# Optimization experiments

Measured on AMD Instinct MI355X. Metric: run time of the kernel, lower is better.

The kernel has to match this reference:

```python
import jax, jax.numpy as jnp
import numpy as np

H = 256   # d_model (SSM copies)
N = 32    # half state size (conjugate symmetry)
S = 256   # n_ssm (trainable copies); repeat = H//S = 1
R = 1     # low-rank correction rank
CCH = 32  # channels; must equal N for the final dC contraction
LMAX = 2048
BATCH = 2


def _r2c(x):
    return x[..., 0] + 1j * x[..., 1]


def setup_inputs() -> dict:
    key = jax.random.key(0)
    ks = jax.random.split(key, 8)
    # dt ~ loguniform(1e-3, 1e-1), standard S4 init
    log_dt = jnp.log(1e-3) + jax.random.uniform(ks[0], (H,), dtype=jnp.float32) * (jnp.log(1e-1) - jnp.log(1e-3))
    B_ri = 0.5 * jax.random.normal(ks[1], (1, S, N, 2), dtype=jnp.float32)
    P_ri = 0.5 * jax.random.normal(ks[2], (R, S, N, 2), dtype=jnp.float32)
    C_ri = 0.5 * jax.random.normal(ks[3], (CCH, H, N, 2), dtype=jnp.float32)
    # real_type='exp': w_real = -exp(inv_w_real) < 0 (stable poles)
    inv_w_real = 0.5 * jax.random.normal(ks[4], (S, N), dtype=jnp.float32)
    # HiPPO-style imaginary parts ~ pi * n, with small noise
    w_imag = jnp.pi * jnp.broadcast_to(jnp.arange(N, dtype=jnp.float32), (S, N)) + 0.01 * jax.random.normal(ks[5], (S, N), dtype=jnp.float32)
    dC = 0.1 * jax.random.normal(ks[6], (LMAX, H, N), dtype=jnp.float32)
    previous_decode = jax.random.normal(ks[7], (BATCH, H, LMAX), dtype=jnp.float32)
    return dict(log_dt=log_dt, B_ri=B_ri, P_ri=P_ri, C_ri=C_ri,
                inv_w_real=inv_w_real, w_imag=w_imag, dC=dC,
                previous_decode=previous_decode, L=LMAX)


def _ss_kernel(log_dt, B_ri, P_ri, C_ri, inv_w_real, w_imag, L):
    """NPLR SSM kernel K_L via Cauchy evaluation + rank-1 Woodbury + irfft. Returns (channels, H, L) real."""
    H_ = log_dt.shape[0]
    S_ = inv_w_real.shape[0]
    rep = H_ // S_
    dt = jnp.exp(log_dt)                              # (H,)
    B = _r2c(B_ri)                                    # (1, S, N)
    P = _r2c(P_ri)                                    # (R, S, N)
    C = _r2c(C_ri)                                    # (CCH, H, N)
    Q = jnp.conj(P)
    w = -jnp.exp(inv_w_real) + 1j * w_imag            # (S, N), real_type='exp'
    # FFT nodes (roots of unity) and bilinear-transformed nodes
    Lf = L // 2 + 1
    omega = jnp.exp((-2j * jnp.pi / L) * jnp.arange(Lf, dtype=jnp.float32))  # (Lf,)
    z = 2 * (1 - omega) / (1 + omega)                 # (Lf,)
    # broadcast S -> H ('r t n -> r (v t) n')
    B = jnp.tile(B, (1, rep, 1))                      # (1, H, N)
    P = jnp.tile(P, (1, rep, 1))                      # (R, H, N)
    Q = jnp.tile(Q, (1, rep, 1))
    w = jnp.tile(w, (rep, 1)) * dt[:, None]           # (H, N) : w * dt
    Bc = jnp.concatenate([B, P], axis=0)              # (1+R, H, N)
    Cc = jnp.concatenate([C, Q], axis=0)              # (CCH+R, H, N)
    v = Bc[:, None] * Cc[None]                        # (1+R, CCH+R, H, N)
    # conjugate-symmetric Cauchy kernel: sum_n v/(z-w) + conj(v)/(z-conj(w))
    cau_p = 1.0 / (z[None, None, :] - w[:, :, None])              # (H, N, Lf)
    cau_m = 1.0 / (z[None, None, :] - jnp.conj(w)[:, :, None])    # (H, N, Lf)
    r = jnp.einsum('ijhn,hnl->ijhl', v, cau_p) + jnp.einsum('ijhn,hnl->ijhl', jnp.conj(v), cau_m)
    r = r * dt[None, None, :, None]
    # rank-1 Woodbury correction
    k_f = r[:-1, :-1] - r[:-1, -1:] * r[-1:, :-1] / (1 + r[-1:, -1:])  # (1, CCH, H, Lf)
    k_f = k_f * 2 / (1 + omega)
    k = jnp.fft.irfft(k_f, n=L, axis=-1)              # (1, CCH, H, L) real
    return k[-1]                                      # (CCH, H, L)


def reference(log_dt, B_ri, P_ri, C_ri, inv_w_real, w_imag, dC, previous_decode, L):
    k = _ss_kernel(log_dt, B_ri, P_ri, C_ri, inv_w_real, w_imag, L)  # (CCH, H, L)
    # FFT convolution of previous_decode with the kernel (length-2L, linear conv)
    k_f = jnp.fft.rfft(k, n=2 * L, axis=-1)                          # (CCH, H, L+1)
    pd_f = jnp.fft.rfft(previous_decode, n=2 * L, axis=-1)           # (B, H, L+1)
    x_f = jnp.einsum('bhl,chl->bhcl', pd_f, k_f)                     # (B, H, CCH, L+1)
    x_pred = jnp.fft.irfft(x_f, n=2 * L, axis=-1)[..., :L]           # (B, H, CCH, L)
    out = jnp.einsum('bhnl,lhn->bhl', x_pred, dC)                    # (B, H, L)
    return out
```

## Files before the change

### kernel.cpp

```cpp
#include <hip/hip_runtime.h>
#include <math.h>

#define LF   1025

#define OFF_ZT   65536
#define OFF_KF   131072
#define OFF_PDF  67371008
#define OFF_DCT  84148224

__device__ __forceinline__ float2 cmulf(float2 a, float2 b){
    return make_float2(a.x*b.x - a.y*b.y, a.x*b.y + a.y*b.x);
}

__device__ __forceinline__ float2 twid(float r){
    float s, c;
    asm("v_sin_f32 %0, %1" : "=v"(s) : "v"(r));
    asm("v_cos_f32 %0, %1" : "=v"(c) : "v"(r));
    return make_float2(c, -s);
}
__device__ __forceinline__ float frcp(float x){
    float y; asm("v_rcp_f32 %0, %1" : "=v"(y) : "v"(x)); return y;
}
__device__ __forceinline__ void lds_fence(){
    asm volatile("s_waitcnt lgkmcnt(0)" ::: "memory");
}

#define GS 548
__device__ __forceinline__ int gslot(int g, int s){ return g*GS + s + (s >> 4); }
__device__ __forceinline__ int binslot(int j){ return gslot(j & 3, j >> 2); }

__global__ void initk(float4* __restrict__ ZT){
    int i = blockIdx.x*256 + threadIdx.x;
    if (i < LF){
        double th = (-2.0*M_PI) * (double)i / 2048.0;
        double cr = cos(th), ci = sin(th);
        double ar = 1.0 + cr, ai = ci;
        double den = ar*ar + ai*ai;
        double nr = 1.0 - cr, ni = -ci;
        double zr = 2.0*(nr*ar + ni*ai)/den;
        double zi = 2.0*(ni*ar - nr*ai)/den;
        ZT[i] = make_float4((float)zr, (float)zi, (float)(2.0*ar/den), (float)(-2.0*ai/den));
    }
}

__global__ __launch_bounds__(256) void transpose_dC(const float* __restrict__ dC, float* __restrict__ DCT){
    __shared__ float tile[32][260];
    int hc0 = blockIdx.x*32;
    int l0  = blockIdx.y*256;
    int tx = threadIdx.x;
    int ty = threadIdx.y;
    for (int li = ty; li < 256; li += 8)
        tile[tx][li] = dC[(size_t)(l0+li)*8192 + hc0 + tx];
    __syncthreads();
    for (int i = ty; i < 32; i += 8){
        #pragma unroll
        for (int pk = 0; pk < 256; pk += 32){
            int po = pk + tx;
            int ll = ((po & 63) << 2) | (po >> 6);
            DCT[(size_t)(hc0+i)*2048 + l0 + po] = tile[i][ll];
        }
    }
}

__global__ __launch_bounds__(256,2) void cauchy_k(
                         const float* __restrict__ log_dt, const float* __restrict__ B_ri,
                         const float* __restrict__ P_ri, const float* __restrict__ C_ri,
                         const float* __restrict__ ivw, const float* __restrict__ wimag,
                         const float4* __restrict__ ZT, float2* __restrict__ KF)
{
    const int h  = blockIdx.y;
    const int c0 = blockIdx.z * 16;
    const int l  = blockIdx.x*256 + (int)threadIdx.x;
    __shared__ float2 wv[32], bv[32], pv[32];
    __shared__ float2 cc[16][32];
    __shared__ float dt_sh;
    if (threadIdx.x < 32){
        int n = threadIdx.x;
        float dt = expf(log_dt[h]);
        wv[n] = make_float2(-expf(ivw[h*32+n]) * dt, wimag[h*32+n] * dt);
        bv[n] = make_float2(B_ri[(h*32+n)*2+0], B_ri[(h*32+n)*2+1]);
        pv[n] = make_float2(P_ri[(h*32+n)*2+0], P_ri[(h*32+n)*2+1]);
        if (n == 0) dt_sh = dt;
    }
    #pragma unroll
    for (int k2 = 0; k2 < 2; ++k2){
        int i = threadIdx.x + k2*256;
        int cj = i >> 5, n = i & 31;
        size_t base = (((size_t)(c0+cj)*256 + h)*32 + n)*2;
        cc[cj][n] = make_float2(C_ri[base+0], C_ri[base+1]);
    }
    __syncthreads();
    if (l >= LF) return;

    float4 zt = ZT[l];
    const float zx = zt.x, zy = zt.y;
    float r0x[17], r0y[17], r1x[17], r1y[17];
    #pragma unroll
    for (int j=0;j<17;++j){ r0x[j]=0.f; r0y[j]=0.f; r1x[j]=0.f; r1y[j]=0.f; }

    #pragma unroll 1
    for (int n=0; n<32; ++n){
        float2 wn = wv[n];
        float dx = zx - wn.x;
        float dy = zy - wn.y;
        float ey = zy + wn.y;
        float ip = frcp(dx*dx + dy*dy);
        float im = frcp(dx*dx + ey*ey);
        float cpx = dx*ip, cpy = -dy*ip;
        float cmx = dx*im, cmy = -ey*im;
        float2 bn = bv[n];
        float br = bn.x, bi = bn.y;
        float t0x = br*cpx - bi*cpy, t0y = br*cpy + bi*cpx;
        float t1x = br*cmx + bi*cmy, t1y = br*cmy - bi*cmx;
        float2 pn = pv[n];
        float pr = pn.x, pi = pn.y;
        float t2x = pr*cpx - pi*cpy, t2y = pr*cpy + pi*cpx;
        float t3x = pr*cmx + pi*cmy, t3y = pr*cmy - pi*cmx;
        float u0 = t0x+t1x, v0 = t1y-t0y, s0 = t0y+t1y, q0 = t0x-t1x;
        float u1 = t2x+t3x, v1 = t3y-t2y, s1 = t2y+t3y, q1 = t2x-t3x;
        r0x[16] = fmaf(pr,u0, fmaf(-pi,v0, r0x[16]));
        r0y[16] = fmaf(pr,s0, fmaf(-pi,q0, r0y[16]));
        r1x[16] = fmaf(pr,u1, fmaf(-pi,v1, r1x[16]));
        r1y[16] = fmaf(pr,s1, fmaf(-pi,q1, r1y[16]));
        #pragma unroll
        for (int j=0;j<16;++j){
            float2 c = cc[j][n];
            float a = c.x, b = c.y;
            r0x[j] = fmaf(a,u0, fmaf(b,v0, r0x[j]));
            r0y[j] = fmaf(a,s0, fmaf(b,q0, r0y[j]));
            r1x[j] = fmaf(a,u1, fmaf(b,v1, r1x[j]));
            r1y[j] = fmaf(a,s1, fmaf(b,q1, r1y[j]));
        }
    }

    float dt = dt_sh;
    #pragma unroll
    for (int j=0;j<17;++j){ r0x[j]*=dt; r0y[j]*=dt; r1x[j]*=dt; r1y[j]*=dt; }
    float drr = 1.0f + r1x[16], dii = r1y[16];
    float idn = frcp(drr*drr + dii*dii);
    float gx = (r0x[16]*drr + r0y[16]*dii)*idn;
    float gy = (r0y[16]*drr - r0x[16]*dii)*idn;
    float tfx = zt.z, tfy = zt.w;
    #pragma unroll
    for (int j=0;j<16;++j){
        float kr = r0x[j] - (gx*r1x[j] - gy*r1y[j]);
        float ki = r0y[j] - (gx*r1y[j] + gy*r1x[j]);
        KF[((size_t)((c0+j)*256+h))*1026 + l] = make_float2(kr*tfx - ki*tfy, kr*tfy + ki*tfx);
    }
}

template<bool INV>
__device__ __forceinline__ void bfly8(float2 v[8]){
    float2 e0,e1,e2,e3,o0,o1,o2,o3;
    {
        float t0x=v[0].x+v[4].x, t0y=v[0].y+v[4].y;
        float t1x=v[0].x-v[4].x, t1y=v[0].y-v[4].y;
        float t2x=v[2].x+v[6].x, t2y=v[2].y+v[6].y;
        float t3x=v[2].x-v[6].x, t3y=v[2].y-v[6].y;
        e0 = make_float2(t0x+t2x, t0y+t2y);
        e2 = make_float2(t0x-t2x, t0y-t2y);
        if (!INV){ e1 = make_float2(t1x+t3y, t1y-t3x); e3 = make_float2(t1x-t3y, t1y+t3x); }
        else     { e1 = make_float2(t1x-t3y, t1y+t3x); e3 = make_float2(t1x+t3y, t1y-t3x); }
    }
    {
        float t0x=v[1].x+v[5].x, t0y=v[1].y+v[5].y;
        float t1x=v[1].x-v[5].x, t1y=v[1].y-v[5].y;
        float t2x=v[3].x+v[7].x, t2y=v[3].y+v[7].y;
        float t3x=v[3].x-v[7].x, t3y=v[3].y-v[7].y;
        o0 = make_float2(t0x+t2x, t0y+t2y);
        o2 = make_float2(t0x-t2x, t0y-t2y);
        if (!INV){ o1 = make_float2(t1x+t3y, t1y-t3x); o3 = make_float2(t1x-t3y, t1y+t3x); }
        else     { o1 = make_float2(t1x-t3y, t1y+t3x); o3 = make_float2(t1x+t3y, t1y-t3x); }
    }
    const float RC = 0.70710678118654752f;
    float2 w1o1, w2o2, w3o3;
    if (!INV){
        w1o1 = make_float2(RC*(o1.x+o1.y), RC*(o1.y-o1.x));
        w2o2 = make_float2(o2.y, -o2.x);
        w3o3 = make_float2(RC*(o3.y-o3.x), RC*(-o3.x-o3.y));
    } else {
        w1o1 = make_float2(RC*(o1.x-o1.y), RC*(o1.y+o1.x));
        w2o2 = make_float2(-o2.y, o2.x);
        w3o3 = make_float2(RC*(-o3.x-o3.y), RC*(o3.x-o3.y));
    }
    v[0] = make_float2(e0.x+o0.x,   e0.y+o0.y);
    v[1] = make_float2(e1.x+w1o1.x, e1.y+w1o1.y);
    v[2] = make_float2(e2.x+w2o2.x, e2.y+w2o2.y);
    v[3] = make_float2(e3.x+w3o3.x, e3.y+w3o3.y);
    v[4] = make_float2(e0.x-o0.x,   e0.y-o0.y);
    v[5] = make_float2(e1.x-w1o1.x, e1.y-w1o1.y);
    v[6] = make_float2(e2.x-w2o2.x, e2.y-w2o2.y);
    v[7] = make_float2(e3.x-w3o3.x, e3.y-w3o3.y);
}

template<bool INV, bool REGOUT>
__device__ __forceinline__ void fftR(float2 v[8], int r0, float2* __restrict__ A, float2* __restrict__ B){
    const int t = threadIdx.x;
    #pragma unroll
    for (int half=0; half<2; ++half){
        int r = r0 + half*256;
        float2 x0=v[half], x1=v[2+half], x2=v[4+half], x3=v[6+half];
        float t0x=x0.x+x2.x, t0y=x0.y+x2.y;
        float t1x=x0.x-x2.x, t1y=x0.y-x2.y;
        float t2x=x1.x+x3.x, t2y=x1.y+x3.y;
        float t3x=x1.x-x3.x, t3y=x1.y-x3.y;
        float2 y0 = make_float2(t0x+t2x, t0y+t2y);
        float2 y2 = make_float2(t0x-t2x, t0y-t2y);
        float2 y1, y3;
        if (!INV){ y1 = make_float2(t1x+t3y, t1y-t3x); y3 = make_float2(t1x-t3y, t1y+t3x); }
        else     { y1 = make_float2(t1x-t3y, t1y+t3x); y3 = make_float2(t1x+t3y, t1y-t3x); }
        float2 w1 = twid((float)r * (1.0f/2048.0f));
        if (INV) w1.y = -w1.y;
        float2 w2 = cmulf(w1,w1);
        float2 w3 = cmulf(w2,w1);
        A[gslot(0,r)] = y0;
        A[gslot(1,r)] = cmulf(y1,w1);
        A[gslot(2,r)] = cmulf(y2,w2);
        A[gslot(3,r)] = cmulf(y3,w3);
    }
    __syncthreads();
    const int w = t >> 6, l = t & 63;
    {
        float2 u[8];
        #pragma unroll
        for (int m=0;m<8;++m) u[m] = A[gslot(w, l + 64*m)];
        bfly8<INV>(u);
        #pragma unroll
        for (int q=0;q<8;++q) B[gslot(w, 8*l+q)] = u[q];
    }
    lds_fence();
    {
        float2 u[8];
        #pragma unroll
        for (int m=0;m<8;++m) u[m] = B[gslot(w, l + 64*m)];
        int jm = l & 7;
        float2 w1 = twid((float)jm * (1.0f/64.0f));
        if (INV) w1.y = -w1.y;
        float2 wc = w1;
        #pragma unroll
        for (int m=1;m<8;++m){ u[m] = cmulf(u[m], wc); if (m<7) wc = cmulf(wc, w1); }
        bfly8<INV>(u);
        int d = ((l - jm) << 3) + jm;
        #pragma unroll
        for (int q=0;q<8;++q) A[gslot(w, d + q*8)] = u[q];
    }
    lds_fence();
    {
        float2 u[8];
        #pragma unroll
        for (int m=0;m<8;++m) u[m] = A[gslot(w, l + 64*m)];
        float2 w1 = twid((float)l * (1.0f/512.0f));
        if (INV) w1.y = -w1.y;
        float2 wc = w1;
        #pragma unroll
        for (int m=1;m<8;++m){ u[m] = cmulf(u[m], wc); if (m<7) wc = cmulf(wc, w1); }
        bfly8<INV>(u);
        if constexpr (REGOUT){
            #pragma unroll
            for (int q=0;q<8;++q) v[q] = u[q];
        } else {
            #pragma unroll
            for (int q=0;q<8;++q) B[gslot(w, l + q*64)] = u[q];
        }
    }
    __syncthreads();
}

__global__ __launch_bounds__(256,2) void kernC2(const float* __restrict__ pd,
                                                float2* __restrict__ PDE, float2* __restrict__ PDO){
    __shared__ float2 A[4*GS], Bb[4*GS];
    const int t = threadIdx.x;
    const int h = blockIdx.x;
    const float* p0 = pd + (size_t)h * 2048;
    const float* p1 = pd + (size_t)(256 + h) * 2048;
    float2 z[8], v[8];
    #pragma unroll
    for (int m=0;m<8;++m){
        int j = t + m*256;
        z[m] = make_float2(p0[j], p1[j]);
        v[m] = z[m];
    }
    fftR<false,false>(v, t, A, Bb);
    float2* oe = PDE + (size_t)h * 2048;
    #pragma unroll
    for (int m=0;m<8;++m){ int j = t + m*256; oe[j] = Bb[binslot(j)]; }
    #pragma unroll
    for (int m=0;m<8;++m){
        int j = t + m*256;
        v[m] = cmulf(twid((float)j * (1.0f/4096.0f)), z[m]);
    }
    fftR<false,false>(v, t, A, Bb);
    float2* oo = PDO + (size_t)h * 2048;
    #pragma unroll
    for (int m=0;m<8;++m){ int j = t + m*256; oo[j] = Bb[binslot(j)]; }
}

__global__ __launch_bounds__(256,2) void kernF(const float2* __restrict__ KFb,
                                               const float2* __restrict__ PDE,
                                               const float2* __restrict__ PDO,
                                               const float* __restrict__ DCT,
                                               float* __restrict__ out){
    __shared__ float2 A[4*GS], Bb[4*GS];
    __shared__ float2 pde_s[2048], pdo_s[2048];
    const int t = threadIdx.x;
    const int h = blockIdx.x;
    const int cq = blockIdx.y;
    const int jbase = ((t & 63) << 2) | (t >> 6);
    {
        const float2* pe = PDE + (size_t)h * 2048;
        const float2* po = PDO + (size_t)h * 2048;
        #pragma unroll
        for (int m=0;m<8;++m){
            int j = t + m*256;
            pde_s[j] = pe[j];
            pdo_s[j] = po[j];
        }
    }
    float accr[8], acci[8];
    #pragma unroll
    for (int m=0;m<8;++m){ accr[m]=0.f; acci[m]=0.f; }
    __syncthreads();

    #pragma unroll 1
    for (int pp=0; pp<8; ++pp){
        const int ca = cq*16 + pp*2;
        const float2* ra = KFb + (size_t)(ca*256+h)*1026;
        const float2* rb = KFb + (size_t)((ca+1)*256+h)*1026;

        float dcva[8], dcvb[8];
        {
            const float* dcta = DCT + (size_t)(h*32 + ca) * 2048;
            const float* dctb = dcta + 2048;
            #pragma unroll
            for (int m=0;m<8;++m){
                int j = t + m*256;
                dcva[m] = dcta[j] * (1.0f/4096.0f);
                dcvb[m] = dctb[j] * (1.0f/4096.0f);
            }
        }
        float2 v[8];

        #pragma unroll
        for (int m=0;m<8;++m){
            int j = t + m*256;
            float2 u;
            if (j <= 1024) u = ra[j];
            else { float2 w = ra[2048-j]; u = make_float2(w.x, -w.y); }
            v[m] = cmulf(pde_s[j], u);
        }
        fftR<true,true>(v, t, A, Bb);
        #pragma unroll
        for (int m=0;m<8;++m){
            accr[m] = fmaf(v[m].x, dcva[m], accr[m]);
            acci[m] = fmaf(v[m].y, dcva[m], acci[m]);
        }
        #pragma unroll
        for (int m=0;m<8;++m){
            int j = t + m*256;
            float2 u;
            if (j <= 1024) u = rb[j];
            else { float2 w = rb[2048-j]; u = make_float2(w.x, -w.y); }
            v[m] = cmulf(pde_s[j], u);
        }
        fftR<true,true>(v, t, A, Bb);
        #pragma unroll
        for (int m=0;m<8;++m){
            accr[m] = fmaf(v[m].x, dcvb[m], accr[m]);
            acci[m] = fmaf(v[m].y, dcvb[m], acci[m]);
        }

        #pragma unroll
        for (int m=0;m<8;++m){
            int j = t + m*256;
            float2 va, vb;
            if (j <= 1024){ va = ra[j]; vb = rb[j]; }
            else {
                float2 u = ra[2048-j]; va = make_float2(u.x, -u.y);
                float2 w = rb[2048-j]; vb = make_float2(w.x, -w.y);
            }
            v[m] = make_float2(va.x - vb.y, va.y + vb.x);
        }
        fftR<true,true>(v, t, A, Bb);
        #pragma unroll
        for (int m=0;m<8;++m){
            float2 kk = v[m];
            kk.x *= (1.0f/2048.0f); kk.y *= (1.0f/2048.0f);
            v[m] = cmulf(kk, twid((float)(jbase + 256*m) * (1.0f/4096.0f)));
        }
        fftR<false,false>(v, jbase, A, Bb);

        float2 pa[8], sb[8];
        #pragma unroll
        for (int m=0;m<8;++m){
            int j  = t + m*256;
            float2 z  = Bb[binslot(j)];
            float2 zm = Bb[binslot(2047 - j)];
            float2 Ka = make_float2(0.5f*(z.x + zm.x), 0.5f*(z.y - zm.y));
            float2 Kb = make_float2(0.5f*(z.y + zm.y), 0.5f*(zm.x - z.x));
            float2 pov = pdo_s[j];
            pa[m] = cmulf(pov, Ka);
            sb[m] = cmulf(pov, Kb);
        }
        fftR<true,true>(pa, t, A, Bb);
        #pragma unroll
        for (int m=0;m<8;++m){
            float2 w = twid((float)(jbase + 256*m) * (1.0f/4096.0f));
            float2 ee = make_float2(w.x, -w.y);
            float2 rot = cmulf(ee, pa[m]);
            accr[m] = fmaf(rot.x, dcva[m], accr[m]);
            acci[m] = fmaf(rot.y, dcva[m], acci[m]);
        }
        fftR<true,true>(sb, t, A, Bb);
        #pragma unroll
        for (int m=0;m<8;++m){
            float2 w = twid((float)(jbase + 256*m) * (1.0f/4096.0f));
            float2 ee = make_float2(w.x, -w.y);
            float2 rot = cmulf(ee, sb[m]);
            accr[m] = fmaf(rot.x, dcvb[m], accr[m]);
            acci[m] = fmaf(rot.y, dcvb[m], acci[m]);
        }
    }
    #pragma unroll
    for (int m=0;m<8;++m){
        int jq = jbase + 256*m;
        atomicAdd(&out[((size_t)h)*2048 + jq],       accr[m]);
        atomicAdd(&out[((size_t)(256+h))*2048 + jq], acci[m]);
    }
}

extern "C" void kernel_launch(void* const* d_in, const int* in_sizes, int n_in,
                              void* d_out, int out_size, void* d_ws, size_t ws_size,
                              hipStream_t stream) {
    const float* log_dt = (const float*)d_in[0];
    const float* B_ri   = (const float*)d_in[1];
    const float* P_ri   = (const float*)d_in[2];
    const float* C_ri   = (const float*)d_in[3];
    const float* ivw    = (const float*)d_in[4];
    const float* wimag  = (const float*)d_in[5];
    const float* dC     = (const float*)d_in[6];
    const float* pd     = (const float*)d_in[7];

    char* ws = (char*)d_ws;
    float4* ZT  = (float4*)(ws + OFF_ZT);
    float2* KF  = (float2*)(ws + OFF_KF);
    float2* PDE = (float2*)(ws + OFF_PDF);
    float2* PDO = (float2*)(ws + OFF_PDF + 256*2048*sizeof(float2));
    float*  DCT = (float*) (ws + OFF_DCT);
    float* out = (float*)d_out;

    hipMemsetAsync(out, 0, (size_t)out_size * sizeof(float), stream);
    initk<<<5, 256, 0, stream>>>(ZT);
    transpose_dC<<<dim3(256,8), dim3(32,8), 0, stream>>>(dC, DCT);
    cauchy_k<<<dim3(5,256,2), 256, 0, stream>>>(log_dt, B_ri, P_ri, C_ri, ivw, wimag, ZT, KF);
    kernC2<<<256, 256, 0, stream>>>(pd, PDE, PDO);
    kernF<<<dim3(256,2), 256, 0, stream>>>((const float2*)KF, PDE, PDO, DCT, out);
}
```

Before: 366.1 us.

## Fuse node table into cauchy kernel and input FFT into final kernel

Removes the initk launch by computing the bilinear nodes and scale factor in double precision inside cauchy_k per thread, and removes kernC2 by doing the forward FFTs of previous_decode inside kernF, writing them straight to shared memory. This drops two kernel launches and the global round trip of the PDE/PDO spectra. In exchange, each of the two cq blocks per h now repeats the input FFT, and every cauchy thread does double-precision cos/sin/div work, which is slow on the GPU.

After: 372.0 us. No clear change (+1.6%).

```diff
diff --git a/kernel.cpp b/kernel.cpp
--- a/kernel.cpp
+++ b/kernel.cpp
@@ -3,9 +3,7 @@
 
 #define LF   1025
 
-#define OFF_ZT   65536
 #define OFF_KF   131072
-#define OFF_PDF  67371008
 #define OFF_DCT  84148224
 
 __device__ __forceinline__ float2 cmulf(float2 a, float2 b){
@@ -28,20 +26,6 @@
 #define GS 548
 __device__ __forceinline__ int gslot(int g, int s){ return g*GS + s + (s >> 4); }
 __device__ __forceinline__ int binslot(int j){ return gslot(j & 3, j >> 2); }
-
-__global__ void initk(float4* __restrict__ ZT){
-    int i = blockIdx.x*256 + threadIdx.x;
-    if (i < LF){
-        double th = (-2.0*M_PI) * (double)i / 2048.0;
-        double cr = cos(th), ci = sin(th);
-        double ar = 1.0 + cr, ai = ci;
-        double den = ar*ar + ai*ai;
-        double nr = 1.0 - cr, ni = -ci;
-        double zr = 2.0*(nr*ar + ni*ai)/den;
-        double zi = 2.0*(ni*ar - nr*ai)/den;
-        ZT[i] = make_float4((float)zr, (float)zi, (float)(2.0*ar/den), (float)(-2.0*ai/den));
-    }
-}
 
 __global__ __launch_bounds__(256) void transpose_dC(const float* __restrict__ dC, float* __restrict__ DCT){
     __shared__ float tile[32][260];
@@ -66,7 +50,7 @@
                          const float* __restrict__ log_dt, const float* __restrict__ B_ri,
                          const float* __restrict__ P_ri, const float* __restrict__ C_ri,
                          const float* __restrict__ ivw, const float* __restrict__ wimag,
-                         const float4* __restrict__ ZT, float2* __restrict__ KF)
+                         float2* __restrict__ KF)
 {
     const int h  = blockIdx.y;
     const int c0 = blockIdx.z * 16;
@@ -92,8 +76,18 @@
     __syncthreads();
     if (l >= LF) return;
 
-    float4 zt = ZT[l];
-    const float zx = zt.x, zy = zt.y;
+    float zx, zy, tfx, tfy;
+    {
+        double th = (-2.0*M_PI) * (double)l / 2048.0;
+        double cr = cos(th), ci = sin(th);
+        double ar = 1.0 + cr, ai = ci;
+        double den = ar*ar + ai*ai;
+        double nr = 1.0 - cr, ni = -ci;
+        zx  = (float)(2.0*(nr*ar + ni*ai)/den);
+        zy  = (float)(2.0*(ni*ar - nr*ai)/den);
+        tfx = (float)(2.0*ar/den);
+        tfy = (float)(-2.0*ai/den);
+    }
     float r0x[17], r0y[17], r1x[17], r1y[17];
     #pragma unroll
     for (int j=0;j<17;++j){ r0x[j]=0.f; r0y[j]=0.f; r1x[j]=0.f; r1y[j]=0.f; }
@@ -140,7 +134,6 @@
     float idn = frcp(drr*drr + dii*dii);
     float gx = (r0x[16]*drr + r0y[16]*dii)*idn;
     float gy = (r0y[16]*drr - r0x[16]*dii)*idn;
-    float tfx = zt.z, tfy = zt.w;
     #pragma unroll
     for (int j=0;j<16;++j){
         float kr = r0x[j] - (gx*r1x[j] - gy*r1y[j]);
@@ -266,38 +259,8 @@
     __syncthreads();
 }
 
-__global__ __launch_bounds__(256,2) void kernC2(const float* __restrict__ pd,
-                                                float2* __restrict__ PDE, float2* __restrict__ PDO){
-    __shared__ float2 A[4*GS], Bb[4*GS];
-    const int t = threadIdx.x;
-    const int h = blockIdx.x;
-    const float* p0 = pd + (size_t)h * 2048;
-    const float* p1 = pd + (size_t)(256 + h) * 2048;
-    float2 z[8], v[8];
-    #pragma unroll
-    for (int m=0;m<8;++m){
-        int j = t + m*256;
-        z[m] = make_float2(p0[j], p1[j]);
-        v[m] = z[m];
-    }
-    fftR<false,false>(v, t, A, Bb);
-    float2* oe = PDE + (size_t)h * 2048;
-    #pragma unroll
-    for (int m=0;m<8;++m){ int j = t + m*256; oe[j] = Bb[binslot(j)]; }
-    #pragma unroll
-    for (int m=0;m<8;++m){
-        int j = t + m*256;
-        v[m] = cmulf(twid((float)j * (1.0f/4096.0f)), z[m]);
-    }
-    fftR<false,false>(v, t, A, Bb);
-    float2* oo = PDO + (size_t)h * 2048;
-    #pragma unroll
-    for (int m=0;m<8;++m){ int j = t + m*256; oo[j] = Bb[binslot(j)]; }
-}
-
 __global__ __launch_bounds__(256,2) void kernF(const float2* __restrict__ KFb,
-                                               const float2* __restrict__ PDE,
-                                               const float2* __restrict__ PDO,
+                                               const float* __restrict__ pd,
                                                const float* __restrict__ DCT,
                                                float* __restrict__ out){
     __shared__ float2 A[4*GS], Bb[4*GS];
@@ -306,15 +269,28 @@
     const int h = blockIdx.x;
     const int cq = blockIdx.y;
     const int jbase = ((t & 63) << 2) | (t >> 6);
-    {
-        const float2* pe = PDE + (size_t)h * 2048;
-        const float2* po = PDO + (size_t)h * 2048;
+
+    {
+        const float* p0 = pd + (size_t)h * 2048;
+        const float* p1 = pd + (size_t)(256 + h) * 2048;
+        float2 z[8], v[8];
         #pragma unroll
         for (int m=0;m<8;++m){
             int j = t + m*256;
-            pde_s[j] = pe[j];
-            pdo_s[j] = po[j];
-        }
+            z[m] = make_float2(p0[j], p1[j]);
+            v[m] = z[m];
+        }
+        fftR<false,false>(v, t, A, Bb);
+        #pragma unroll
+        for (int m=0;m<8;++m){ int j = t + m*256; pde_s[j] = Bb[binslot(j)]; }
+        #pragma unroll
+        for (int m=0;m<8;++m){
+            int j = t + m*256;
+            v[m] = cmulf(twid((float)j * (1.0f/4096.0f)), z[m]);
+        }
+        fftR<false,false>(v, t, A, Bb);
+        #pragma unroll
+        for (int m=0;m<8;++m){ int j = t + m*256; pdo_s[j] = Bb[binslot(j)]; }
     }
     float accr[8], acci[8];
     #pragma unroll
@@ -441,17 +417,12 @@
     const float* pd     = (const float*)d_in[7];
 
     char* ws = (char*)d_ws;
-    float4* ZT  = (float4*)(ws + OFF_ZT);
     float2* KF  = (float2*)(ws + OFF_KF);
-    float2* PDE = (float2*)(ws + OFF_PDF);
-    float2* PDO = (float2*)(ws + OFF_PDF + 256*2048*sizeof(float2));
     float*  DCT = (float*) (ws + OFF_DCT);
     float* out = (float*)d_out;
 
     hipMemsetAsync(out, 0, (size_t)out_size * sizeof(float), stream);
-    initk<<<5, 256, 0, stream>>>(ZT);
     transpose_dC<<<dim3(256,8), dim3(32,8), 0, stream>>>(dC, DCT);
-    cauchy_k<<<dim3(5,256,2), 256, 0, stream>>>(log_dt, B_ri, P_ri, C_ri, ivw, wimag, ZT, KF);
-    kernC2<<<256, 256, 0, stream>>>(pd, PDE, PDO);
-    kernF<<<dim3(256,2), 256, 0, stream>>>((const float2*)KF, PDE, PDO, DCT, out);
-}
+    cauchy_k<<<dim3(5,256,2), 256, 0, stream>>>(log_dt, B_ri, P_ri, C_ri, ivw, wimag, KF);
+    kernF<<<dim3(256,2), 256, 0, stream>>>((const float2*)KF, pd, DCT, out);
+}
```
